# Kernel optimization log

Hardware: AMD Instinct MI355X
Metric: run time of the kernel (lower is better)

The kernel has to match this reference:

```python
import jax, jax.numpy as jnp
import numpy as np

N = 4096
F_IN = 256
HEADS = 8
FEAT = 64
NEG_SLOPE = 0.2


def setup_inputs() -> dict:
    key = jax.random.key(0)
    k_x, k_adj, k_w, k_s, k_d = jax.random.split(key, 5)
    x = jax.random.normal(k_x, (N, F_IN), dtype=jnp.float32)
    adj = (jax.random.uniform(k_adj, (N, N)) < 0.02).astype(jnp.float32)
    W = jax.random.normal(k_w, (F_IN, HEADS * FEAT), dtype=jnp.float32) * (1.0 / np.sqrt(F_IN))
    a_src = jax.random.normal(k_s, (FEAT,), dtype=jnp.float32) * (1.0 / np.sqrt(FEAT))
    a_dst = jax.random.normal(k_d, (FEAT,), dtype=jnp.float32) * (1.0 / np.sqrt(FEAT))
    return {"x": x, "adj": adj, "W": W, "a_src": a_src, "a_dst": a_dst}


def reference(x, adj, W, a_src, a_dst):
    n = x.shape[0]
    adj = adj + jnp.eye(n, dtype=adj.dtype)          # add self loops
    h = (x @ W).reshape(n, HEADS, FEAT)              # (N, H, F)
    s_src = jnp.einsum('nhf,f->nh', h, a_src)        # (N, H)
    s_dst = jnp.einsum('nhf,f->nh', h, a_dst)        # (N, H)
    # e[i, j, h] = leaky_relu(s_src[i,h] + s_dst[j,h])  -> (N, N, H)
    e = jax.nn.leaky_relu(s_src[:, None, :] + s_dst[None, :, :], negative_slope=NEG_SLOPE)
    mask = (adj == 0)                                # (N, N)
    e = jnp.where(mask[:, :, None], -1e9, e)
    alpha = jax.nn.softmax(e, axis=1)                # softmax over neighbor axis j
    out = jnp.einsum('ijh,jhf->ihf', alpha, h)       # (N, H, F)
    return out.reshape(n, HEADS * FEAT)              # concat heads -> (N, 512)
```

## Files before the change

### kernel.cpp

```cpp
#include <hip/hip_runtime.h>
#include <hip/hip_bf16.h>
#include <hip/hip_fp16.h>
#include <stdint.h>

#define NROWS 4096
#define FIN   256
#define NHEADS 8
#define HF    512
#define NEG   0.2f
#define MAXDEG 160

#define LBAR() do { asm volatile("s_waitcnt lgkmcnt(0)" ::: "memory"); \
                    __builtin_amdgcn_s_barrier(); } while (0)

__global__ __launch_bounds__(256) void k_gemm(const float* __restrict__ x,
                                              const float* __restrict__ W,
                                              const float* __restrict__ a_src,
                                              const float* __restrict__ a_dst,
                                              __half* __restrict__ hfp,
                                              float* __restrict__ s_src,
                                              float* __restrict__ s_dst) {
    __shared__ __align__(16) float As[16][68];
    __shared__ __align__(16) float Bs[16][68];
    const int t  = threadIdx.x;
    const int bm = blockIdx.x >> 3;
    const int bn = blockIdx.x & 7;
    const int ty = t >> 4, tx = t & 15;

    const int am  = t >> 2;
    const int ak4 = (t & 3) << 2;
    const int bk  = t >> 4;
    const int bn4 = (t & 15) << 2;

    float acc[4][4] = {};

    for (int kt = 0; kt < FIN; kt += 16) {
        float4 av = *(const float4*)&x[(size_t)(bm*64 + am)*FIN + kt + ak4];
        float4 bv = *(const float4*)&W[(size_t)(kt + bk)*HF + bn*64 + bn4];
        LBAR();
        As[ak4+0][am] = av.x; As[ak4+1][am] = av.y;
        As[ak4+2][am] = av.z; As[ak4+3][am] = av.w;
        *(float4*)&Bs[bk][bn4] = bv;
        LBAR();
        #pragma unroll
        for (int k = 0; k < 16; ++k) {
            float4 a = *(const float4*)&As[k][ty*4];
            float4 b = *(const float4*)&Bs[k][tx*4];
            float ar[4] = {a.x, a.y, a.z, a.w};
            float br[4] = {b.x, b.y, b.z, b.w};
            #pragma unroll
            for (int r = 0; r < 4; ++r)
                #pragma unroll
                for (int c = 0; c < 4; ++c)
                    acc[r][c] += ar[r] * br[c];
        }
    }

    #pragma unroll
    for (int r = 0; r < 4; ++r) {
        int row = bm*64 + ty*4 + r;
        int col = bn*64 + tx*4;
        __half2* dst = (__half2*)&hfp[(size_t)row*HF + col];
        dst[0] = __floats2half2_rn(acc[r][0], acc[r][1]);
        dst[1] = __floats2half2_rn(acc[r][2], acc[r][3]);
    }

    float4 avs = *(const float4*)&a_src[tx*4];
    float4 avd = *(const float4*)&a_dst[tx*4];
    #pragma unroll
    for (int r = 0; r < 4; ++r) {
        float ps = acc[r][0]*avs.x + acc[r][1]*avs.y + acc[r][2]*avs.z + acc[r][3]*avs.w;
        float pd = acc[r][0]*avd.x + acc[r][1]*avd.y + acc[r][2]*avd.z + acc[r][3]*avd.w;
        #pragma unroll
        for (int msk = 1; msk < 16; msk <<= 1) {
            ps += __shfl_xor(ps, msk);
            pd += __shfl_xor(pd, msk);
        }
        if (tx == 0) {
            int row = bm*64 + ty*4 + r;
            s_src[row*NHEADS + bn] = ps;
            s_dst[row*NHEADS + bn] = pd;
        }
    }
}

__global__ __launch_bounds__(256, 4) void k_agg(const float* __restrict__ adj,
                                                const float* __restrict__ s_src,
                                                const float* __restrict__ s_dst,
                                                const __half* __restrict__ hfp,
                                                float* __restrict__ out) {
    __shared__ float    ebuf[4][NHEADS][164];
    __shared__ uint16_t nbr[4][168];

    const int t = threadIdx.x;
    const int w = t >> 6, lane = t & 63;
    const int row = blockIdx.x * 4 + w;

    const float* ar = adj + (size_t)row * NROWS + lane*4;
    float4 f[16];
    #pragma unroll
    for (int k = 0; k < 16; ++k) f[k] = *(const float4*)(ar + k*256);

    uint64_t pm = 0;
    #pragma unroll
    for (int k = 0; k < 16; ++k) {
        if (f[k].x != 0.f) pm |= 1ull << (k*4+0);
        if (f[k].y != 0.f) pm |= 1ull << (k*4+1);
        if (f[k].z != 0.f) pm |= 1ull << (k*4+2);
        if (f[k].w != 0.f) pm |= 1ull << (k*4+3);
    }
    if (((row >> 2) & 63) == lane)
        pm |= 1ull << (((row >> 8) << 2) | (row & 3));

    int pcnt = __popcll(pm);
    int incl = pcnt;
    #pragma unroll
    for (int d = 1; d < 64; d <<= 1) {
        int u = __shfl_up(incl, d);
        if (lane >= d) incl += u;
    }
    int total = __shfl(incl, 63);
    int pos = incl - pcnt;
    if (total > MAXDEG) total = MAXDEG;

    uint64_t m = pm;
    while (m) {
        int q = (int)__ffsll((unsigned long long)m) - 1;  m &= m - 1;
        int col = ((q >> 2) << 8) + lane*4 + (q & 3);
        if (pos < MAXDEG) nbr[w][pos] = (uint16_t)col;
        pos++;
    }
    __builtin_amdgcn_wave_barrier();

    float4 s0 = *(const float4*)&s_src[row*NHEADS];
    float4 s1 = *(const float4*)&s_src[row*NHEADS + 4];
    for (int p = lane; p < total; p += 64) {
        int j = nbr[w][p];
        float4 d0 = *(const float4*)&s_dst[j*NHEADS];
        float4 d1 = *(const float4*)&s_dst[j*NHEADS + 4];
        float e;
        e = s0.x + d0.x; ebuf[w][0][p] = e > 0.f ? e : NEG*e;
        e = s0.y + d0.y; ebuf[w][1][p] = e > 0.f ? e : NEG*e;
        e = s0.z + d0.z; ebuf[w][2][p] = e > 0.f ? e : NEG*e;
        e = s0.w + d0.w; ebuf[w][3][p] = e > 0.f ? e : NEG*e;
        e = s1.x + d1.x; ebuf[w][4][p] = e > 0.f ? e : NEG*e;
        e = s1.y + d1.y; ebuf[w][5][p] = e > 0.f ? e : NEG*e;
        e = s1.z + d1.z; ebuf[w][6][p] = e > 0.f ? e : NEG*e;
        e = s1.w + d1.w; ebuf[w][7][p] = e > 0.f ? e : NEG*e;
    }
    __builtin_amdgcn_wave_barrier();

    const int hh = lane & 7, idx = lane >> 3;
    float mx = -1e30f;
    for (int p = idx; p < total; p += 8) mx = fmaxf(mx, ebuf[w][hh][p]);
    mx = fmaxf(mx, __shfl_xor(mx, 8));
    mx = fmaxf(mx, __shfl_xor(mx, 16));
    mx = fmaxf(mx, __shfl_xor(mx, 32));

    float ssum = 0.f;
    for (int p = idx; p < total; p += 8) {
        float ev = __expf(ebuf[w][hh][p] - mx);
        ebuf[w][hh][p] = ev;
        ssum += ev;
    }
    ssum += __shfl_xor(ssum, 8);
    ssum += __shfl_xor(ssum, 16);
    ssum += __shfl_xor(ssum, 32);
    float inv = 1.f / ssum;
    __builtin_amdgcn_wave_barrier();

    const int h3 = lane >> 3;
    const float invg = __shfl(inv, h3);
    const uint4* hb4 = (const uint4*)hfp;
    float c0=0,c1=0,c2=0,c3=0,c4=0,c5=0,c6=0,c7=0;

    const int T4 = (total + 3) & ~3;
    for (int p = 0; p < T4; p += 4) {
        const int p1 = p+1, p2 = p+2, p3 = p+3;
        const int o1 = p1 < total, o2 = p2 < total, o3 = p3 < total;
        int j0 = nbr[w][p];
        int j1 = nbr[w][o1 ? p1 : 0];
        int j2 = nbr[w][o2 ? p2 : 0];
        int j3 = nbr[w][o3 ? p3 : 0];
        float a0 = ebuf[w][h3][p];
        float a1 = o1 ? ebuf[w][h3][p1] : 0.f;
        float a2 = o2 ? ebuf[w][h3][p2] : 0.f;
        float a3 = o3 ? ebuf[w][h3][p3] : 0.f;
        uint4 v0 = hb4[(size_t)j0*64 + lane];
        uint4 v1 = hb4[(size_t)j1*64 + lane];
        uint4 v2 = hb4[(size_t)j2*64 + lane];
        uint4 v3 = hb4[(size_t)j3*64 + lane];
        union { uint4 u; __half h[8]; } U0, U1, U2, U3;
        U0.u = v0; U1.u = v1; U2.u = v2; U3.u = v3;
        c0 += __half2float(U0.h[0])*a0; c1 += __half2float(U0.h[1])*a0;
        c2 += __half2float(U0.h[2])*a0; c3 += __half2float(U0.h[3])*a0;
        c4 += __half2float(U0.h[4])*a0; c5 += __half2float(U0.h[5])*a0;
        c6 += __half2float(U0.h[6])*a0; c7 += __half2float(U0.h[7])*a0;
        c0 += __half2float(U1.h[0])*a1; c1 += __half2float(U1.h[1])*a1;
        c2 += __half2float(U1.h[2])*a1; c3 += __half2float(U1.h[3])*a1;
        c4 += __half2float(U1.h[4])*a1; c5 += __half2float(U1.h[5])*a1;
        c6 += __half2float(U1.h[6])*a1; c7 += __half2float(U1.h[7])*a1;
        c0 += __half2float(U2.h[0])*a2; c1 += __half2float(U2.h[1])*a2;
        c2 += __half2float(U2.h[2])*a2; c3 += __half2float(U2.h[3])*a2;
        c4 += __half2float(U2.h[4])*a2; c5 += __half2float(U2.h[5])*a2;
        c6 += __half2float(U2.h[6])*a2; c7 += __half2float(U2.h[7])*a2;
        c0 += __half2float(U3.h[0])*a3; c1 += __half2float(U3.h[1])*a3;
        c2 += __half2float(U3.h[2])*a3; c3 += __half2float(U3.h[3])*a3;
        c4 += __half2float(U3.h[4])*a3; c5 += __half2float(U3.h[5])*a3;
        c6 += __half2float(U3.h[6])*a3; c7 += __half2float(U3.h[7])*a3;
    }

    float* orow = out + (size_t)row*HF + lane*8;
    *(float4*)(orow)     = make_float4(c0*invg, c1*invg, c2*invg, c3*invg);
    *(float4*)(orow + 4) = make_float4(c4*invg, c5*invg, c6*invg, c7*invg);
}

extern "C" void kernel_launch(void* const* d_in, const int* in_sizes, int n_in,
                              void* d_out, int out_size, void* d_ws, size_t ws_size,
                              hipStream_t stream) {
    const float* x     = (const float*)d_in[0];
    const float* adj   = (const float*)d_in[1];
    const float* W     = (const float*)d_in[2];
    const float* a_src = (const float*)d_in[3];
    const float* a_dst = (const float*)d_in[4];
    float* out = (float*)d_out;

    char* ws = (char*)d_ws;
    __half* hfp   = (__half*)ws;
    float*  s_src = (float*)(ws + 4u*1024*1024);
    float*  s_dst = (float*)(ws + 4u*1024*1024 + 128u*1024);

    k_gemm<<<512,  256, 0, stream>>>(x, W, a_src, a_dst, hfp, s_src, s_dst);
    k_agg <<<1024, 256, 0, stream>>>(adj, s_src, s_dst, hfp, out);
}
```

Before: 53.85 us.

## Split each aggregation row across two waves by head half

Each output row is now handled by two waves, one per group of four heads, instead of one wave covering all eight heads. The grid doubles and the occupancy hint rises to 8 blocks per CU. The neighbor gather loop now unrolls by 8 with half-width loads, and the neighbor list is padded with zeros to a multiple of 8 so the loop needs no bounds checks. This trades more wave-level parallelism and more loads in flight against both waves rescanning the same dense adjacency row, plus register pressure under the tighter launch bound, which may cause spills of the 16-float4 adjacency buffer.

```diff
diff --git a/kernel.cpp b/kernel.cpp
--- a/kernel.cpp
+++ b/kernel.cpp
@@ -84,17 +84,18 @@
     }
 }
 
-__global__ __launch_bounds__(256, 4) void k_agg(const float* __restrict__ adj,
+__global__ __launch_bounds__(256, 8) void k_agg(const float* __restrict__ adj,
                                                 const float* __restrict__ s_src,
                                                 const float* __restrict__ s_dst,
                                                 const __half* __restrict__ hfp,
                                                 float* __restrict__ out) {
-    __shared__ float    ebuf[4][NHEADS][164];
+    __shared__ float    ebuf[4][4][168];
     __shared__ uint16_t nbr[4][168];
 
     const int t = threadIdx.x;
     const int w = t >> 6, lane = t & 63;
-    const int row = blockIdx.x * 4 + w;
+    const int row  = blockIdx.x * 2 + (w >> 1);
+    const int half = w & 1;
 
     const float* ar = adj + (size_t)row * NROWS + lane*4;
     float4 f[16];
@@ -122,6 +123,7 @@
     int total = __shfl(incl, 63);
     int pos = incl - pcnt;
     if (total > MAXDEG) total = MAXDEG;
+    const int T8 = (total + 7) & ~7;
 
     uint64_t m = pm;
     while (m) {
@@ -130,89 +132,76 @@
         if (pos < MAXDEG) nbr[w][pos] = (uint16_t)col;
         pos++;
     }
+    for (int p = total + lane; p < T8; p += 64) nbr[w][p] = 0;
     __builtin_amdgcn_wave_barrier();
 
-    float4 s0 = *(const float4*)&s_src[row*NHEADS];
-    float4 s1 = *(const float4*)&s_src[row*NHEADS + 4];
-    for (int p = lane; p < total; p += 64) {
-        int j = nbr[w][p];
-        float4 d0 = *(const float4*)&s_dst[j*NHEADS];
-        float4 d1 = *(const float4*)&s_dst[j*NHEADS + 4];
-        float e;
-        e = s0.x + d0.x; ebuf[w][0][p] = e > 0.f ? e : NEG*e;
-        e = s0.y + d0.y; ebuf[w][1][p] = e > 0.f ? e : NEG*e;
-        e = s0.z + d0.z; ebuf[w][2][p] = e > 0.f ? e : NEG*e;
-        e = s0.w + d0.w; ebuf[w][3][p] = e > 0.f ? e : NEG*e;
-        e = s1.x + d1.x; ebuf[w][4][p] = e > 0.f ? e : NEG*e;
-        e = s1.y + d1.y; ebuf[w][5][p] = e > 0.f ? e : NEG*e;
-        e = s1.z + d1.z; ebuf[w][6][p] = e > 0.f ? e : NEG*e;
-        e = s1.w + d1.w; ebuf[w][7][p] = e > 0.f ? e : NEG*e;
+    float4 s = *(const float4*)&s_src[row*NHEADS + half*4];
+    for (int p = lane; p < T8; p += 64) {
+        if (p < total) {
+            int j = nbr[w][p];
+            float4 d = *(const float4*)&s_dst[j*NHEADS + half*4];
+            float e;
+            e = s.x + d.x; ebuf[w][0][p] = e > 0.f ? e : NEG*e;
+            e = s.y + d.y; ebuf[w][1][p] = e > 0.f ? e : NEG*e;
+            e = s.z + d.z; ebuf[w][2][p] = e > 0.f ? e : NEG*e;
+            e = s.w + d.w; ebuf[w][3][p] = e > 0.f ? e : NEG*e;
+        } else {
+            ebuf[w][0][p] = 0.f; ebuf[w][1][p] = 0.f;
+            ebuf[w][2][p] = 0.f; ebuf[w][3][p] = 0.f;
+        }
     }
     __builtin_amdgcn_wave_barrier();
 
-    const int hh = lane & 7, idx = lane >> 3;
+    const int hh = lane & 3, idx = lane >> 2;
     float mx = -1e30f;
-    for (int p = idx; p < total; p += 8) mx = fmaxf(mx, ebuf[w][hh][p]);
+    for (int p = idx; p < total; p += 16) mx = fmaxf(mx, ebuf[w][hh][p]);
+    mx = fmaxf(mx, __shfl_xor(mx, 4));
     mx = fmaxf(mx, __shfl_xor(mx, 8));
     mx = fmaxf(mx, __shfl_xor(mx, 16));
     mx = fmaxf(mx, __shfl_xor(mx, 32));
 
     float ssum = 0.f;
-    for (int p = idx; p < total; p += 8) {
+    for (int p = idx; p < total; p += 16) {
         float ev = __expf(ebuf[w][hh][p] - mx);
         ebuf[w][hh][p] = ev;
         ssum += ev;
     }
+    ssum += __shfl_xor(ssum, 4);
     ssum += __shfl_xor(ssum, 8);
     ssum += __shfl_xor(ssum, 16);
     ssum += __shfl_xor(ssum, 32);
     float inv = 1.f / ssum;
     __builtin_amdgcn_wave_barrier();
 
-    const int h3 = lane >> 3;
+    const int h3 = lane >> 4;
     const float invg = __shfl(inv, h3);
-    const uint4* hb4 = (const uint4*)hfp;
-    float c0=0,c1=0,c2=0,c3=0,c4=0,c5=0,c6=0,c7=0;
-
-    const int T4 = (total + 3) & ~3;
-    for (int p = 0; p < T4; p += 4) {
-        const int p1 = p+1, p2 = p+2, p3 = p+3;
-        const int o1 = p1 < total, o2 = p2 < total, o3 = p3 < total;
-        int j0 = nbr[w][p];
-        int j1 = nbr[w][o1 ? p1 : 0];
-        int j2 = nbr[w][o2 ? p2 : 0];
-        int j3 = nbr[w][o3 ? p3 : 0];
-        float a0 = ebuf[w][h3][p];
-        float a1 = o1 ? ebuf[w][h3][p1] : 0.f;
-        float a2 = o2 ? ebuf[w][h3][p2] : 0.f;
-        float a3 = o3 ? ebuf[w][h3][p3] : 0.f;
-        uint4 v0 = hb4[(size_t)j0*64 + lane];
-        uint4 v1 = hb4[(size_t)j1*64 + lane];
-        uint4 v2 = hb4[(size_t)j2*64 + lane];
-        uint4 v3 = hb4[(size_t)j3*64 + lane];
-        union { uint4 u; __half h[8]; } U0, U1, U2, U3;
-        U0.u = v0; U1.u = v1; U2.u = v2; U3.u = v3;
-        c0 += __half2float(U0.h[0])*a0; c1 += __half2float(U0.h[1])*a0;
-        c2 += __half2float(U0.h[2])*a0; c3 += __half2float(U0.h[3])*a0;
-        c4 += __half2float(U0.h[4])*a0; c5 += __half2float(U0.h[5])*a0;
-        c6 += __half2float(U0.h[6])*a0; c7 += __half2float(U0.h[7])*a0;
-        c0 += __half2float(U1.h[0])*a1; c1 += __half2float(U1.h[1])*a1;
-        c2 += __half2float(U1.h[2])*a1; c3 += __half2float(U1.h[3])*a1;
-        c4 += __half2float(U1.h[4])*a1; c5 += __half2float(U1.h[5])*a1;
-        c6 += __half2float(U1.h[6])*a1; c7 += __half2float(U1.h[7])*a1;
-        c0 += __half2float(U2.h[0])*a2; c1 += __half2float(U2.h[1])*a2;
-        c2 += __half2float(U2.h[2])*a2; c3 += __half2float(U2.h[3])*a2;
-        c4 += __half2float(U2.h[4])*a2; c5 += __half2float(U2.h[5])*a2;
-        c6 += __half2float(U2.h[6])*a2; c7 += __half2float(U2.h[7])*a2;
-        c0 += __half2float(U3.h[0])*a3; c1 += __half2float(U3.h[1])*a3;
-        c2 += __half2float(U3.h[2])*a3; c3 += __half2float(U3.h[3])*a3;
-        c4 += __half2float(U3.h[4])*a3; c5 += __half2float(U3.h[5])*a3;
-        c6 += __half2float(U3.h[6])*a3; c7 += __half2float(U3.h[7])*a3;
-    }
-
-    float* orow = out + (size_t)row*HF + lane*8;
-    *(float4*)(orow)     = make_float4(c0*invg, c1*invg, c2*invg, c3*invg);
-    *(float4*)(orow + 4) = make_float4(c4*invg, c5*invg, c6*invg, c7*invg);
+    const uint2* hb2 = (const uint2*)hfp;
+    const int lidx = half*64 + lane;
+    float c0 = 0.f, c1 = 0.f, c2 = 0.f, c3 = 0.f;
+
+    for (int p = 0; p < T8; p += 8) {
+        int   jj[8];
+        uint2 vv[8];
+        float aa[8];
+        #pragma unroll
+        for (int u = 0; u < 8; ++u) jj[u] = nbr[w][p + u];
+        #pragma unroll
+        for (int u = 0; u < 8; ++u) vv[u] = hb2[(size_t)jj[u]*128 + lidx];
+        #pragma unroll
+        for (int u = 0; u < 8; ++u) aa[u] = ebuf[w][h3][p + u];
+        #pragma unroll
+        for (int u = 0; u < 8; ++u) {
+            union { uint2 u2; __half h[4]; } U;
+            U.u2 = vv[u];
+            c0 += __half2float(U.h[0]) * aa[u];
+            c1 += __half2float(U.h[1]) * aa[u];
+            c2 += __half2float(U.h[2]) * aa[u];
+            c3 += __half2float(U.h[3]) * aa[u];
+        }
+    }
+
+    *(float4*)&out[(size_t)row*HF + half*256 + lane*4] =
+        make_float4(c0*invg, c1*invg, c2*invg, c3*invg);
 }
 
 extern "C" void kernel_launch(void* const* d_in, const int* in_sizes, int n_in,
@@ -231,5 +220,5 @@
     float*  s_dst = (float*)(ws + 4u*1024*1024 + 128u*1024);
 
     k_gemm<<<512,  256, 0, stream>>>(x, W, a_src, a_dst, hfp, s_src, s_dst);
-    k_agg <<<1024, 256, 0, stream>>>(adj, s_src, s_dst, hfp, out);
+    k_agg <<<2048, 256, 0, stream>>>(adj, s_src, s_dst, hfp, out);
 }
```

Measured after the change: 57.91 us. 7.5% more time.
